# Kernel optimization log

Measured on AMD Instinct MI355X. Metric: run time of the kernel, lower is better.

Reference implementation:

```python
import jax, jax.numpy as jnp
import numpy as np
import math

EMBED_DIM = 1024
NUM_HEADS = 16
D_K = EMBED_DIM // NUM_HEADS  # 64 qubits per head
BATCH, SEQ = 4, 2048


def setup_inputs() -> dict:
    key = jax.random.key(0)
    k_x, k_th, k_w, k_b = jax.random.split(key, 4)
    x = jax.random.normal(k_x, (BATCH, SEQ, EMBED_DIM), dtype=jnp.float32)
    # trainable RX angle per head per qubit (tq.RX has one param each)
    theta = jax.random.normal(k_th, (NUM_HEADS, D_K), dtype=jnp.float32)
    # out_linear
    lim = 1.0 / math.sqrt(EMBED_DIM)
    w_out = jax.random.uniform(k_w, (EMBED_DIM, EMBED_DIM), jnp.float32, -lim, lim)
    b_out = jax.random.uniform(k_b, (EMBED_DIM,), jnp.float32, -lim, lim)
    return {"x": x, "theta": theta, "w_out": w_out, "b_out": b_out}


def reference(x, theta, w_out, b_out):
    B, S, E = x.shape
    H, d_k = theta.shape
    # Quantum head: RX(x_i) then RX(theta_i) on |0>, measure PauliZ ->
    # <Z_i> = cos(x_i + theta_i). No entangling gates in the code path.
    ang = x.reshape(B, S, H, d_k) + theta  # broadcast [H,d_k]
    qkv = jnp.cos(ang).transpose(0, 2, 1, 3)  # [B,H,S,d_k]; Q == K == V
    scale = 1.0 / math.sqrt(d_k)
    scores = jnp.einsum('bhqd,bhkd->bhqk', qkv, qkv) * scale
    attn = jax.nn.softmax(scores, axis=-1)  # dropout is identity in eval
    out = jnp.einsum('bhqk,bhkd->bhqd', attn, qkv)
    out = out.transpose(0, 2, 1, 3).reshape(B, S, E)
    return out @ w_out.T + b_out
```

## Files before the change

kernel.cpp:

```cpp
#include <hip/hip_runtime.h>


#define B_  4
#define S_  2048
#define H_  16
#define D_  64
#define E_  1024
#define EXP2_SCALE 0.18033688011112043f

typedef unsigned short u16;
typedef unsigned int u32;
typedef __attribute__((ext_vector_type(8))) short short8;
typedef __attribute__((ext_vector_type(4))) float floatx4;

static __device__ __forceinline__ float bf2f(u16 v) {
    return __uint_as_float(((unsigned)v) << 16);
}
static __device__ __forceinline__ u16 f2bf(float f) {
    unsigned u = __float_as_uint(f);
    return (u16)((u + 0x7FFFu + ((u >> 16) & 1u)) >> 16);
}
static __device__ __forceinline__ u32 pack_bf16_trunc(float lo, float hi) {
    return __builtin_amdgcn_perm(__float_as_uint(hi), __float_as_uint(lo), 0x07060302u);
}
static __device__ __forceinline__ short8 scale8(short8 v) {
    short8 o;
#pragma unroll
    for (int i = 0; i < 8; i++)
        o[i] = (short)f2bf(bf2f((u16)v[i]) * EXP2_SCALE);
    return o;
}

#define KSWZ(r, c) ((((r)) << 6) + (((c) ^ ((((r)) & 7) << 3))))

__global__ __launch_bounds__(256) void prep_kernel(const float* __restrict__ x,
                                                   const float* __restrict__ theta,
                                                   const float* __restrict__ W,
                                                   u16* __restrict__ qkv,
                                                   u16* __restrict__ qkvT,
                                                   u16* __restrict__ Wb) {
    __shared__ __align__(16) u16 TQ[64][72];
    int blk = blockIdx.x;
    int tid = threadIdx.x;
    if (blk >= 2048) {
        int i = ((blk - 2048) * 256 + tid) * 4;
        float4 w = *(const float4*)(W + i);
        ushort4 o;
        o.x = f2bf(w.x); o.y = f2bf(w.y); o.z = f2bf(w.z); o.w = f2bf(w.w);
        *(ushort4*)(Wb + i) = o;
        return;
    }
    int stile = blk & 31;
    int bh    = blk >> 5;
    int b     = bh >> 4;
    int h     = bh & 15;
    int i     = tid >> 2;
    int d0    = (tid & 3) << 4;
    int s0    = stile << 6;
    int s     = s0 + i;

    const float* xp = x + ((size_t)(b * S_ + s)) * E_ + h * D_ + d0;
    const float* tp = theta + h * D_ + d0;

    u16 ov[16];
#pragma unroll
    for (int j = 0; j < 16; j += 4) {
        float4 xv = *(const float4*)(xp + j);
        float4 tv = *(const float4*)(tp + j);
        ov[j]     = f2bf(__cosf(xv.x + tv.x));
        ov[j + 1] = f2bf(__cosf(xv.y + tv.y));
        ov[j + 2] = f2bf(__cosf(xv.z + tv.z));
        ov[j + 3] = f2bf(__cosf(xv.w + tv.w));
    }

    u16* qp = qkv + ((size_t)bh * S_ + s) * D_ + d0;
    *(uint4*)qp       = *(uint4*)&ov[0];
    *(uint4*)(qp + 8) = *(uint4*)&ov[8];

#pragma unroll
    for (int j = 0; j < 16; j++) TQ[d0 + j][i] = ov[j];
    __syncthreads();

    int d  = tid >> 2;
    int j0 = (tid & 3) << 4;
    u16 tmp[16];
#pragma unroll
    for (int j = 0; j < 16; j++) tmp[j] = TQ[d][j0 + j];
    u16* qtp = qkvT + ((size_t)bh * D_ + d) * S_ + s0 + j0;
    *(uint4*)qtp       = *(uint4*)&tmp[0];
    *(uint4*)(qtp + 8) = *(uint4*)&tmp[8];
}

__global__ __launch_bounds__(256, 4) void attn_kernel(const u16* __restrict__ qkv,
                                                      const u16* __restrict__ qkvT,
                                                      u16* __restrict__ aout) {
    int blk0 = blockIdx.x;
    int blk  = (blk0 & 7) * 128 + (blk0 >> 3);
    int qt   = blk & 15;
    int bh   = blk >> 4;
    int b    = bh >> 4;
    int h    = bh & 15;
    int tid  = threadIdx.x;
    int wave = tid >> 6;
    int lane = tid & 63;
    int lq   = lane & 15;
    int lg   = lane >> 4;
    int r    = tid >> 2;
    int c0   = (tid & 3) << 4;

    __shared__ __align__(16) u16 Kt[64 * 64];
    __shared__ __align__(16) u16 Vt[64 * 64];

    const u16* base  = qkv  + (size_t)bh * S_ * D_;
    const u16* baseT = qkvT + (size_t)bh * D_ * S_;
    int s0 = qt * 128;

    short8 bq[2][2];
#pragma unroll
    for (int rf = 0; rf < 2; rf++) {
        const u16* qrow = base + (size_t)(s0 + wave * 32 + rf * 16 + lq) * D_ + lg * 8;
        bq[rf][0] = scale8(*(const short8*)qrow);
        bq[rf][1] = scale8(*(const short8*)(qrow + 32));
    }

    floatx4 oacc[2][4] = {{{0,0,0,0},{0,0,0,0},{0,0,0,0},{0,0,0,0}},
                          {{0,0,0,0},{0,0,0,0},{0,0,0,0},{0,0,0,0}}};
    float lsum[2] = {0.f, 0.f};

    {
        const u16* p = base + (size_t)r * D_ + c0;
        *(uint4*)&Kt[KSWZ(r, c0)]     = *(const uint4*)p;
        *(uint4*)&Kt[KSWZ(r, c0 + 8)] = *(const uint4*)(p + 8);
        const u16* p2 = baseT + (size_t)r * S_ + c0;
        *(uint4*)&Vt[KSWZ(r, c0)]     = *(const uint4*)p2;
        *(uint4*)&Vt[KSWZ(r, c0 + 8)] = *(const uint4*)(p2 + 8);
    }
    __syncthreads();

    for (int kt = 0; kt < S_ / 64; kt++) {
        uint4 bw[2][2];
        u32 pvx[2], pvy[2];
#pragma unroll
        for (int t = 0; t < 4; t++) {
            short8 a0 = *(short8*)&Kt[KSWZ(t * 16 + lq, lg * 8)];
            short8 a1 = *(short8*)&Kt[KSWZ(t * 16 + lq, 32 + lg * 8)];
            floatx4 sct[2];
#pragma unroll
            for (int rf = 0; rf < 2; rf++) {
                floatx4 acc = {0, 0, 0, 0};
                acc = __builtin_amdgcn_mfma_f32_16x16x32_bf16(a0, bq[rf][0], acc, 0, 0, 0);
                sct[rf] = __builtin_amdgcn_mfma_f32_16x16x32_bf16(a1, bq[rf][1], acc, 0, 0, 0);
            }
#pragma unroll
            for (int rf = 0; rf < 2; rf++) {
                float p0 = __builtin_amdgcn_exp2f(sct[rf][0]);
                float p1 = __builtin_amdgcn_exp2f(sct[rf][1]);
                float p2 = __builtin_amdgcn_exp2f(sct[rf][2]);
                float p3 = __builtin_amdgcn_exp2f(sct[rf][3]);
                lsum[rf] += (p0 + p1) + (p2 + p3);
                u32 wx = pack_bf16_trunc(p0, p1);
                u32 wy = pack_bf16_trunc(p2, p3);
                if ((t & 1) == 0) {
                    pvx[rf] = wx;
                    pvy[rf] = wy;
                } else {
                    u32 d0x = pvx[rf], d1x = wx;
                    asm("v_permlane32_swap_b32 %0, %1" : "+v"(d0x), "+v"(d1x));
                    asm("v_permlane16_swap_b32 %0, %1" : "+v"(d0x), "+v"(d1x));
                    u32 d0y = pvy[rf], d1y = wy;
                    asm("v_permlane32_swap_b32 %0, %1" : "+v"(d0y), "+v"(d1y));
                    asm("v_permlane16_swap_b32 %0, %1" : "+v"(d0y), "+v"(d1y));
                    bw[rf][t >> 1] = (uint4){d0x, d0y, d1x, d1y};
                }
            }
        }

        __builtin_amdgcn_s_setprio(1);
#pragma unroll
        for (int t = 0; t < 4; t++) {
            short8 av0 = *(short8*)&Vt[KSWZ(t * 16 + lq, lg * 8)];
            short8 av1 = *(short8*)&Vt[KSWZ(t * 16 + lq, 32 + lg * 8)];
#pragma unroll
            for (int rf = 0; rf < 2; rf++) {
                short8 bp0 = __builtin_bit_cast(short8, bw[rf][0]);
                short8 bp1 = __builtin_bit_cast(short8, bw[rf][1]);
                oacc[rf][t] = __builtin_amdgcn_mfma_f32_16x16x32_bf16(av0, bp0, oacc[rf][t], 0, 0, 0);
                oacc[rf][t] = __builtin_amdgcn_mfma_f32_16x16x32_bf16(av1, bp1, oacc[rf][t], 0, 0, 0);
            }
        }
        __builtin_amdgcn_s_setprio(0);

        __syncthreads();
        if (kt < S_ / 64 - 1) {
            const u16* p = base + (size_t)((kt + 1) * 64 + r) * D_ + c0;
            uint4 k0 = *(const uint4*)p;
            uint4 k1 = *(const uint4*)(p + 8);
            const u16* p2 = baseT + (size_t)r * S_ + (kt + 1) * 64 + c0;
            uint4 v0 = *(const uint4*)p2;
            uint4 v1 = *(const uint4*)(p2 + 8);
            *(uint4*)&Kt[KSWZ(r, c0)]     = k0;
            *(uint4*)&Kt[KSWZ(r, c0 + 8)] = k1;
            *(uint4*)&Vt[KSWZ(r, c0)]     = v0;
            *(uint4*)&Vt[KSWZ(r, c0 + 8)] = v1;
        }
        __syncthreads();
    }

#pragma unroll
    for (int rf = 0; rf < 2; rf++) {
        lsum[rf] += __shfl_xor(lsum[rf], 16);
        lsum[rf] += __shfl_xor(lsum[rf], 32);
    }
#pragma unroll
    for (int rf = 0; rf < 2; rf++) {
        float inv = 1.0f / fmaxf(lsum[rf], 1e-20f);
        int srow = s0 + wave * 32 + rf * 16 + lq;
        u16* arow = aout + ((size_t)(b * S_ + srow)) * E_ + h * D_;
#pragma unroll
        for (int t = 0; t < 4; t++)
#pragma unroll
            for (int rr = 0; rr < 4; rr++)
                arow[t * 16 + lg * 4 + rr] = f2bf(oacc[rf][t][rr] * inv);
    }
}

__global__ __launch_bounds__(256) void proj_kernel(const u16* __restrict__ A,
                                                   const u16* __restrict__ Wb,
                                                   const float* __restrict__ bias,
                                                   float* __restrict__ out) {
    int m0   = blockIdx.x * 128;
    int n0   = blockIdx.y * 128;
    int tid  = threadIdx.x;
    int wave = tid >> 6;
    int wm   = wave >> 1;
    int wn   = wave & 1;
    int lane = tid & 63;
    int lq   = lane & 15;
    int lg   = lane >> 4;
    int r    = tid >> 1;
    int c0   = (tid & 1) * 32;

    __shared__ __align__(16) u16 As[128][72];
    __shared__ __align__(16) u16 Bs[128][72];

    floatx4 acc[4][4];
#pragma unroll
    for (int i = 0; i < 4; i++)
#pragma unroll
        for (int j = 0; j < 4; j++) acc[i][j] = (floatx4){0, 0, 0, 0};

    for (int kc = 0; kc < E_; kc += 64) {
        __syncthreads();
        const u16* pa = A + (size_t)(m0 + r) * E_ + kc + c0;
        const u16* pw = Wb + (size_t)(n0 + r) * E_ + kc + c0;
#pragma unroll
        for (int j = 0; j < 4; j++) {
            *(uint4*)&As[r][c0 + j * 8] = *(const uint4*)(pa + j * 8);
            *(uint4*)&Bs[r][c0 + j * 8] = *(const uint4*)(pw + j * 8);
        }
        __syncthreads();

#pragma unroll
        for (int c = 0; c < 2; c++) {
            short8 af[4], bf[4];
#pragma unroll
            for (int i = 0; i < 4; i++)
                af[i] = *(short8*)&As[wm * 64 + i * 16 + lq][c * 32 + lg * 8];
#pragma unroll
            for (int j = 0; j < 4; j++)
                bf[j] = *(short8*)&Bs[wn * 64 + j * 16 + lq][c * 32 + lg * 8];
#pragma unroll
            for (int i = 0; i < 4; i++)
#pragma unroll
                for (int j = 0; j < 4; j++)
                    acc[i][j] = __builtin_amdgcn_mfma_f32_16x16x32_bf16(af[i], bf[j], acc[i][j], 0, 0, 0);
        }
    }

#pragma unroll
    for (int j = 0; j < 4; j++) {
        int nidx = n0 + wn * 64 + j * 16 + lq;
        float bv = bias[nidx];
#pragma unroll
        for (int i = 0; i < 4; i++) {
#pragma unroll
            for (int rr = 0; rr < 4; rr++) {
                int row = m0 + wm * 64 + i * 16 + lg * 4 + rr;
                out[(size_t)row * E_ + nidx] = acc[i][j][rr] + bv;
            }
        }
    }
}

extern "C" void kernel_launch(void* const* d_in, const int* in_sizes, int n_in,
                              void* d_out, int out_size, void* d_ws, size_t ws_size,
                              hipStream_t stream) {
    const float* x     = (const float*)d_in[0];
    const float* theta = (const float*)d_in[1];
    const float* w_out = (const float*)d_in[2];
    const float* b_out = (const float*)d_in[3];
    float* out = (float*)d_out;

    char* ws = (char*)d_ws;
    const size_t QKV_BYTES = (size_t)B_ * H_ * S_ * D_ * sizeof(u16);
    u16* qkv  = (u16*)ws;
    u16* qkvT = (u16*)(ws + QKV_BYTES);
    u16* aout = (u16*)(ws + 2 * QKV_BYTES);
    u16* wbf_safe = (u16*)(ws + 3 * QKV_BYTES);

    prep_kernel<<<3072, 256, 0, stream>>>(x, theta, w_out, qkv, qkvT, wbf_safe);
    attn_kernel<<<(B_ * H_) * (S_ / 128), 256, 0, stream>>>(qkv, qkvT, aout);
    dim3 pg(B_ * S_ / 128, E_ / 128);
    proj_kernel<<<pg, 256, 0, stream>>>(aout, wbf_safe, b_out, out);
}
```

Measured before the change: 188.2 us.

## Double-buffer K/V tiles in LDS and prefetch next tile into registers

Splits the K and V shared-memory tiles into two buffers and issues the global loads for the next key tile at the start of each iteration, before the QK and PV MFMA work. The loaded values are written to the alternate buffer after compute, which removes one of the two block barriers per iteration and hides global-load latency behind math. The cost is double the LDS footprint (32 KB per block) and extra live registers for the prefetched data, which may reduce occupancy at 4 blocks per CU.

```diff
diff --git a/kernel.cpp b/kernel.cpp
--- a/kernel.cpp
+++ b/kernel.cpp
@@ -108,8 +108,8 @@
     int r    = tid >> 2;
     int c0   = (tid & 3) << 4;
 
-    __shared__ __align__(16) u16 Kt[64 * 64];
-    __shared__ __align__(16) u16 Vt[64 * 64];
+    __shared__ __align__(16) u16 Kt[2][64 * 64];
+    __shared__ __align__(16) u16 Vt[2][64 * 64];
 
     const u16* base  = qkv  + (size_t)bh * S_ * D_;
     const u16* baseT = qkvT + (size_t)bh * D_ * S_;
@@ -129,21 +129,32 @@
 
     {
         const u16* p = base + (size_t)r * D_ + c0;
-        *(uint4*)&Kt[KSWZ(r, c0)]     = *(const uint4*)p;
-        *(uint4*)&Kt[KSWZ(r, c0 + 8)] = *(const uint4*)(p + 8);
+        *(uint4*)&Kt[0][KSWZ(r, c0)]     = *(const uint4*)p;
+        *(uint4*)&Kt[0][KSWZ(r, c0 + 8)] = *(const uint4*)(p + 8);
         const u16* p2 = baseT + (size_t)r * S_ + c0;
-        *(uint4*)&Vt[KSWZ(r, c0)]     = *(const uint4*)p2;
-        *(uint4*)&Vt[KSWZ(r, c0 + 8)] = *(const uint4*)(p2 + 8);
+        *(uint4*)&Vt[0][KSWZ(r, c0)]     = *(const uint4*)p2;
+        *(uint4*)&Vt[0][KSWZ(r, c0 + 8)] = *(const uint4*)(p2 + 8);
     }
     __syncthreads();
 
     for (int kt = 0; kt < S_ / 64; kt++) {
+        int cur = kt & 1;
+        uint4 nk0, nk1, nv0, nv1;
+        if (kt < S_ / 64 - 1) {
+            const u16* p = base + (size_t)((kt + 1) * 64 + r) * D_ + c0;
+            nk0 = *(const uint4*)p;
+            nk1 = *(const uint4*)(p + 8);
+            const u16* p2 = baseT + (size_t)r * S_ + (kt + 1) * 64 + c0;
+            nv0 = *(const uint4*)p2;
+            nv1 = *(const uint4*)(p2 + 8);
+        }
+
         uint4 bw[2][2];
         u32 pvx[2], pvy[2];
 #pragma unroll
         for (int t = 0; t < 4; t++) {
-            short8 a0 = *(short8*)&Kt[KSWZ(t * 16 + lq, lg * 8)];
-            short8 a1 = *(short8*)&Kt[KSWZ(t * 16 + lq, 32 + lg * 8)];
+            short8 a0 = *(short8*)&Kt[cur][KSWZ(t * 16 + lq, lg * 8)];
+            short8 a1 = *(short8*)&Kt[cur][KSWZ(t * 16 + lq, 32 + lg * 8)];
             floatx4 sct[2];
 #pragma unroll
             for (int rf = 0; rf < 2; rf++) {
@@ -178,8 +189,8 @@
         __builtin_amdgcn_s_setprio(1);
 #pragma unroll
         for (int t = 0; t < 4; t++) {
-            short8 av0 = *(short8*)&Vt[KSWZ(t * 16 + lq, lg * 8)];
-            short8 av1 = *(short8*)&Vt[KSWZ(t * 16 + lq, 32 + lg * 8)];
+            short8 av0 = *(short8*)&Vt[cur][KSWZ(t * 16 + lq, lg * 8)];
+            short8 av1 = *(short8*)&Vt[cur][KSWZ(t * 16 + lq, 32 + lg * 8)];
 #pragma unroll
             for (int rf = 0; rf < 2; rf++) {
                 short8 bp0 = __builtin_bit_cast(short8, bw[rf][0]);
@@ -190,18 +201,12 @@
         }
         __builtin_amdgcn_s_setprio(0);
 
-        __syncthreads();
         if (kt < S_ / 64 - 1) {
-            const u16* p = base + (size_t)((kt + 1) * 64 + r) * D_ + c0;
-            uint4 k0 = *(const uint4*)p;
-            uint4 k1 = *(const uint4*)(p + 8);
-            const u16* p2 = baseT + (size_t)r * S_ + (kt + 1) * 64 + c0;
-            uint4 v0 = *(const uint4*)p2;
-            uint4 v1 = *(const uint4*)(p2 + 8);
-            *(uint4*)&Kt[KSWZ(r, c0)]     = k0;
-            *(uint4*)&Kt[KSWZ(r, c0 + 8)] = k1;
-            *(uint4*)&Vt[KSWZ(r, c0)]     = v0;
-            *(uint4*)&Vt[KSWZ(r, c0 + 8)] = v1;
+            int nxt = cur ^ 1;
+            *(uint4*)&Kt[nxt][KSWZ(r, c0)]     = nk0;
+            *(uint4*)&Kt[nxt][KSWZ(r, c0 + 8)] = nk1;
+            *(uint4*)&Vt[nxt][KSWZ(r, c0)]     = nv0;
+            *(uint4*)&Vt[nxt][KSWZ(r, c0 + 8)] = nv1;
         }
         __syncthreads();
     }
```

After: 196.0 us. 1.04x slower.
